# Optimization experiments

Hardware: AMD Instinct MI355X
Metric: run time of the kernel (lower is better)

## Reference

```python
import jax, jax.numpy as jnp
import numpy as np

D_MODEL = 2048
NUM_HEADS = 16
D_K = D_MODEL // NUM_HEADS


def setup_inputs() -> dict:
    key = jax.random.key(0)
    ks = jax.random.split(key, 9)
    s = 1.0 / np.sqrt(D_MODEL)
    x = jax.random.normal(ks[0], (4, 4096, D_MODEL), dtype=jnp.float32)
    wq = jax.random.uniform(ks[1], (D_MODEL, D_MODEL), jnp.float32, -s, s)
    bq = jax.random.uniform(ks[2], (D_MODEL,), jnp.float32, -s, s)
    wk = jax.random.uniform(ks[3], (D_MODEL, D_MODEL), jnp.float32, -s, s)
    bk = jax.random.uniform(ks[4], (D_MODEL,), jnp.float32, -s, s)
    wv = jax.random.uniform(ks[5], (D_MODEL, D_MODEL), jnp.float32, -s, s)
    bv = jax.random.uniform(ks[6], (D_MODEL,), jnp.float32, -s, s)
    wo = jax.random.uniform(ks[7], (D_MODEL, D_MODEL), jnp.float32, -s, s)
    bo = jax.random.uniform(ks[8], (D_MODEL,), jnp.float32, -s, s)
    return {"x": x, "wq": wq, "bq": bq, "wk": wk, "bk": bk,
            "wv": wv, "bv": bv, "wo": wo, "bo": bo}


def _heads(t, B, S):
    # (B, S, d_model) -> (B, H, S, d_k)
    return t.reshape(B, S, NUM_HEADS, D_K).transpose(0, 2, 1, 3)


def reference(x, wq, bq, wk, bk, wv, bv, wo, bo):
    B, S, _ = x.shape
    Q = _heads(x @ wq.T + bq, B, S)
    K = _heads(x @ wk.T + bk, B, S)
    V = _heads(x @ wv.T + bv, B, S)
    # elu(x)+1 feature map
    Q = jax.nn.elu(Q) + 1.0
    K = jax.nn.elu(K) + 1.0
    # KV: (B,H,d_k,d_k)
    KV = jnp.einsum('bhsd,bhse->bhde', K, V)
    QKV = jnp.einsum('bhsd,bhde->bhse', Q, KV)
    K_sum = jnp.sum(K, axis=-2)                      # (B,H,d_k)
    QK_sum = jnp.einsum('bhsd,bhd->bhs', Q, K_sum)   # (B,H,S)
    out = QKV / (QK_sum[..., None] + 1e-8)
    out = out.transpose(0, 2, 1, 3).reshape(B, S, D_MODEL)
    return out @ wo.T + bo
```

## Files before the change

### kernel.cpp

```cpp
#include <hip/hip_runtime.h>


#define D_MODEL 2048
#define SEQ     4096
#define BATCH   4
#define HEADS   16
#define DKH     128
#define M_TOK   16384
#define NBH     64

using frag8 = __attribute__((ext_vector_type(8))) short;
using f32x4 = __attribute__((ext_vector_type(4))) float;

typedef __attribute__((address_space(1))) const unsigned int g_u32;
typedef __attribute__((address_space(3))) unsigned int       l_u32;

__device__ __forceinline__ unsigned short f2bf(float f) {
  unsigned u = __float_as_uint(f);
  u = u + 0x7fffu + ((u >> 16) & 1u);
  return (unsigned short)(u >> 16);
}
__device__ __forceinline__ float bf2f(unsigned short h) {
  return __uint_as_float(((unsigned)h) << 16);
}

__global__ __launch_bounds__(256) void convert_f2bf_kernel(
    const float* __restrict__ in, unsigned short* __restrict__ out, int n4) {
  int i = blockIdx.x * 256 + threadIdx.x;
  if (i < n4) {
    float4 v = reinterpret_cast<const float4*>(in)[i];
    ushort4 o;
    o.x = f2bf(v.x); o.y = f2bf(v.y); o.z = f2bf(v.z); o.w = f2bf(v.w);
    reinterpret_cast<ushort4*>(out)[i] = o;
  }
}


#define ST_B(GB, LD, SLOT, KC)                                                \
  _Pragma("unroll") for (int j_ = 0; j_ < 2; ++j_)                            \
    __builtin_amdgcn_global_load_lds(                                         \
        (g_u32*)((GB) + (srow + wid * 16 + j_ * 8 + (lane >> 3)) * (LD)       \
                 + (KC) + scg * 8),                                           \
        (l_u32*)(sh + (SLOT) * 16384 + 8192 + (wid * 16 + j_ * 8) * 64),      \
        16, 0, 0);

#define ST_A(GA, LD, SP, ST, KC)                                              \
    __builtin_amdgcn_global_load_lds(                                         \
        (g_u32*)((GA) + (srow + (ST) * 32 + (wid & 3) * 8 + (lane >> 3)) * (LD) \
                 + (KC) + (wid >> 2) * 32 + scg * 8),                         \
        (l_u32*)(sh + ((SP) + (wid >> 2)) * 16384 +                           \
                 ((ST) * 32 + (wid & 3) * 8) * 64),                           \
        16, 0, 0);

#define RD_A(S0, S1, Q)                                                       \
  a0[0] = *(const frag8*)(lds + (S0) * 16384 + tA + (Q) * 2048);              \
  a0[1] = *(const frag8*)(lds + (S0) * 16384 + tA + (Q) * 2048 + 1024);       \
  a1[0] = *(const frag8*)(lds + (S1) * 16384 + tA + (Q) * 2048);              \
  a1[1] = *(const frag8*)(lds + (S1) * 16384 + tA + (Q) * 2048 + 1024);

#define RD_B(D0, D1, S0, S1)                                                  \
  _Pragma("unroll") for (int n_ = 0; n_ < 4; ++n_) {                          \
    D0[n_] = *(const frag8*)(lds + (S0) * 16384 + tB + n_ * 1024);            \
    D1[n_] = *(const frag8*)(lds + (S1) * 16384 + tB + n_ * 1024);            \
  }

#define MM8(AQ, B0, B1)                                                       \
  __builtin_amdgcn_s_setprio(1);                                              \
  _Pragma("unroll") for (int j_ = 0; j_ < 2; ++j_)                            \
  _Pragma("unroll") for (int n_ = 0; n_ < 4; ++n_)                            \
    acc[(AQ) + j_][n_] = __builtin_amdgcn_mfma_f32_16x16x32_bf16(             \
        a0[j_], B0[n_], acc[(AQ) + j_][n_], 0, 0, 0);                         \
  _Pragma("unroll") for (int j_ = 0; j_ < 2; ++j_)                            \
  _Pragma("unroll") for (int n_ = 0; n_ < 4; ++n_)                            \
    acc[(AQ) + j_][n_] = __builtin_amdgcn_mfma_f32_16x16x32_bf16(             \
        a1[j_], B1[n_], acc[(AQ) + j_][n_], 0, 0, 0);                         \
  __builtin_amdgcn_s_setprio(0);

#define BAR __builtin_amdgcn_s_barrier()
#define LG0                                                                   \
  asm volatile("s_waitcnt lgkmcnt(0)" ::: "memory");                          \
  __builtin_amdgcn_sched_barrier(0)

template <int MODE, bool XMAJOR>
__global__ __launch_bounds__(512, 2) void gemm256_nt_kernel(
    const unsigned short* __restrict__ A, long lda,
    const unsigned short* __restrict__ Bm, long ldb,
    void* __restrict__ Cv, long ldc,
    const float* __restrict__ bias, float* __restrict__ aux,
    float* __restrict__ qsum, int K) {
  __shared__ unsigned short sh[65536];
  const int lane = threadIdx.x & 63, wid = threadIdx.x >> 6;
  const int wm = wid >> 2, wn = wid & 3;
  const int lr = lane & 15, lh = lane >> 4;

  const int gx = gridDim.x, gy = gridDim.y;
  const int cpx = (gx * gy) >> 3;
  const int P = blockIdx.y * gx + blockIdx.x;
  const int Lw = (P & 7) * cpx + (P >> 3);
  int bx, by;
  if (XMAJOR) { bx = Lw / gy; by = Lw - bx * gy; }
  else        { by = Lw / gx; bx = Lw - by * gx; }

  const long m0 = (long)by * 256, n0 = (long)bx * 256;
  const unsigned short* Ablk = A + m0 * lda;
  const unsigned short* Bblk = Bm + n0 * ldb;
  const int NT = K >> 6;

  const int qA = (wm * 4 + lh) ^ (lr & 7);
  const int qB = ((wn >> 1) * 4 + lh) ^ (lr & 7);
  const unsigned short* lds = sh;
  const int tA = lr * 64 + qA * 8;
  const int tB = 8192 + ((wn & 1) * 64 + lr) * 64 + qB * 8;

  const int sqd = (lane & 7) ^ (lane >> 3);
  const int scg = sqd & 3;
  const long srow = (long)((sqd >> 2) * 128);

  f32x4 acc[8][4];
#pragma unroll
  for (int m = 0; m < 8; ++m)
#pragma unroll
    for (int n = 0; n < 4; ++n) acc[m][n] = (f32x4){0.f, 0.f, 0.f, 0.f};

  frag8 a0[2], a1[2], bu0[4], bu1[4], bv0[4], bv1[4];

  ST_B(Bblk, ldb, 0, 0)
  ST_B(Bblk, ldb, 1, 32)
  ST_A(Ablk, lda, 0, 0, 0) ST_A(Ablk, lda, 0, 1, 0)
  ST_A(Ablk, lda, 0, 2, 0) ST_A(Ablk, lda, 0, 3, 0)
  if (NT > 1) {
    ST_B(Bblk, ldb, 2, 64)
    ST_B(Bblk, ldb, 3, 96)
    ST_A(Ablk, lda, 2, 0, 64) ST_A(Ablk, lda, 2, 1, 64)
  }
  asm volatile("s_waitcnt vmcnt(6)" ::: "memory");
  BAR;

  const int NI = NT >> 1;
  for (int i = 0; i < NI; ++i) {
    const int kv = i * 128 + 64, kw = i * 128 + 128, kx = i * 128 + 192;
    const bool wok = (i + 1) < NI;
    RD_A(0, 1, 0)
    RD_B(bu0, bu1, 0, 1)
    ST_A(Ablk, lda, 2, 2, kv) ST_A(Ablk, lda, 2, 3, kv)
    asm volatile("s_waitcnt lgkmcnt(8)" ::: "memory");
    BAR; LG0;
    MM8(0, bu0, bu1)
    BAR;
    RD_A(0, 1, 1)
    if (wok) { ST_B(Bblk, ldb, 0, kw) }
    BAR; LG0;
    MM8(2, bu0, bu1)
    BAR;
    RD_A(0, 1, 2)
    if (wok) { ST_B(Bblk, ldb, 1, kw + 32) }
    BAR; LG0;
    MM8(4, bu0, bu1)
    BAR;
    RD_A(0, 1, 3)
    if (wok) { ST_A(Ablk, lda, 0, 0, kw) ST_A(Ablk, lda, 0, 1, kw) }
    if (wok) asm volatile("s_waitcnt vmcnt(6)" ::: "memory");
    else     asm volatile("s_waitcnt vmcnt(0)" ::: "memory");
    BAR; LG0;
    MM8(6, bu0, bu1)
    BAR;
    RD_A(2, 3, 0)
    RD_B(bv0, bv1, 2, 3)
    if (wok) { ST_A(Ablk, lda, 0, 2, kw) ST_A(Ablk, lda, 0, 3, kw) }
    asm volatile("s_waitcnt lgkmcnt(8)" ::: "memory");
    BAR; LG0;
    MM8(0, bv0, bv1)
    BAR;
    RD_A(2, 3, 1)
    if (wok) { ST_B(Bblk, ldb, 2, kx) }
    BAR; LG0;
    MM8(2, bv0, bv1)
    BAR;
    RD_A(2, 3, 2)
    if (wok) { ST_B(Bblk, ldb, 3, kx + 32) }
    BAR; LG0;
    MM8(4, bv0, bv1)
    BAR;
    RD_A(2, 3, 3)
    if (wok) { ST_A(Ablk, lda, 2, 0, kx) ST_A(Ablk, lda, 2, 1, kx)
               asm volatile("s_waitcnt vmcnt(6)" ::: "memory"); }
    BAR; LG0;
    MM8(6, bv0, bv1)
    BAR;
  }

  float* red = (float*)sh;
  if (MODE == 0 || MODE == 1) {
    if (threadIdx.x < 512) { red[threadIdx.x] = 0.f; }
    __syncthreads();
  }
  float ksv[4];
  if (MODE == 0) {
    const long b2048 = (m0 >> 12) * 2048;
#pragma unroll
    for (int n = 0; n < 4; ++n)
      ksv[n] = aux[b2048 + n0 + wn * 64 + n * 16 + lr];
  }
#pragma unroll
  for (int m = 0; m < 8; ++m)
#pragma unroll
    for (int r = 0; r < 4; ++r) {
      const int lrow = wm * 128 + (m >> 1) * 32 + (m & 1) * 16 + lh * 4 + r;
      const long row = m0 + lrow;
      float part = 0.f;
#pragma unroll
      for (int n = 0; n < 4; ++n) {
        long col = n0 + wn * 64 + n * 16 + lr;
        float v = acc[m][n][r];
        if (MODE == 0) {
          v += bias[col]; v = v > 0.f ? v + 1.f : __expf(v);
          unsigned short us = f2bf(v);
          ((unsigned short*)Cv)[row * ldc + col] = us;
          part += bf2f(us) * ksv[n];
        } else if (MODE == 1) {
          v += bias[row]; v = v > 0.f ? v + 1.f : __expf(v);
          unsigned short us = f2bf(v);
          ((unsigned short*)Cv)[row * ldc + col] = us;
          part += bf2f(us);
        } else if (MODE == 2) {
          v += bias[row];
          ((unsigned short*)Cv)[row * ldc + col] = f2bf(v);
        } else {
          v += bias[col];
          ((float*)Cv)[row * ldc + col] = v;
        }
      }
      if (MODE == 0 || MODE == 1) {
#pragma unroll
        for (int s = 1; s < 16; s <<= 1) part += __shfl_xor(part, s);
        if (lr == 0) {
          if (MODE == 0) atomicAdd(&red[lrow * 2 + (wn >> 1)], part);
          else           atomicAdd(&red[lrow], part);
        }
      }
    }
  if (MODE == 0) {
    __syncthreads();
    if (threadIdx.x < 512) {
      const int lrow = threadIdx.x >> 1, hh = threadIdx.x & 1;
      const long grow = m0 + lrow;
      qsum[((grow >> 12) * 16 + (n0 >> 7) + hh) * (long)SEQ + (grow & 4095)] =
          red[threadIdx.x];
    }
  } else if (MODE == 1) {
    __syncthreads();
    if (threadIdx.x < 256)
      atomicAdd(&aux[(n0 >> 12) * 2048 + m0 + threadIdx.x], red[threadIdx.x]);
  }
}

__device__ __forceinline__ void stage_tile(const unsigned short* __restrict__ G,
                                           long ld, unsigned short* __restrict__ L) {
  const int w = threadIdx.x >> 6, l = threadIdx.x & 63;
#pragma unroll
  for (int r = 0; r < 4; ++r) {
    const int chunk = w * 4 + r;
    const int row = chunk * 8 + (l >> 3);
    const int col = (l & 7) * 8;
    __builtin_amdgcn_global_load_lds((g_u32*)(G + (long)row * ld + col),
                                     (l_u32*)(L + chunk * 512), 16, 0, 0);
  }
}

__device__ __forceinline__ void gemm_mainloop(const unsigned short* __restrict__ A, long lda,
                                              const unsigned short* __restrict__ B, long ldb,
                                              int K, unsigned short* lA, unsigned short* lB,
                                              f32x4 acc[4][4]) {
  const int lane = threadIdx.x & 63;
  const int wid  = threadIdx.x >> 6;
  const int wr = wid >> 1, wc = wid & 1;
  const int lr = lane & 15, lh = lane >> 4;
  for (int k0 = 0; k0 < K; k0 += 64) {
    stage_tile(A + k0, lda, lA);
    stage_tile(B + k0, ldb, lB);
    __syncthreads();
#pragma unroll
    for (int kk = 0; kk < 64; kk += 32) {
      frag8 av[4], bv[4];
#pragma unroll
      for (int m = 0; m < 4; ++m)
        av[m] = *reinterpret_cast<const frag8*>(lA + (wr * 64 + m * 16 + lr) * 64 + kk + lh * 8);
#pragma unroll
      for (int n = 0; n < 4; ++n)
        bv[n] = *reinterpret_cast<const frag8*>(lB + (wc * 64 + n * 16 + lr) * 64 + kk + lh * 8);
#pragma unroll
      for (int m = 0; m < 4; ++m)
#pragma unroll
        for (int n = 0; n < 4; ++n)
          acc[m][n] = __builtin_amdgcn_mfma_f32_16x16x32_bf16(av[m], bv[n], acc[m][n], 0, 0, 0);
    }
    __syncthreads();
  }
}

#define ACC_INIT(acc)                                   \
  _Pragma("unroll") for (int m_ = 0; m_ < 4; ++m_)      \
  _Pragma("unroll") for (int n_ = 0; n_ < 4; ++n_)      \
      acc[m_][n_] = (f32x4){0.f, 0.f, 0.f, 0.f};

__global__ __launch_bounds__(256) void kvt_partial_kernel(
    const unsigned short* __restrict__ VT, const unsigned short* __restrict__ KT,
    float* __restrict__ part) {
  __shared__ unsigned short lA[128 * 64], lB[128 * 64];
  const int z = blockIdx.x;
  const int bh = z >> 3, c = z & 7;
  const int b = bh >> 4, h = bh & 15;
  const long tOff = (long)b * SEQ + (long)c * 512;
  const unsigned short* A  = VT + (long)(h * DKH) * M_TOK + tOff;
  const unsigned short* Bm = KT + (long)(h * DKH) * M_TOK + tOff;
  f32x4 acc[4][4];
  ACC_INIT(acc);
  gemm_mainloop(A, M_TOK, Bm, M_TOK, 512, lA, lB, acc);
  const int lane = threadIdx.x & 63, wid = threadIdx.x >> 6;
  const int wr = wid >> 1, wc = wid & 1, lr = lane & 15, lh = lane >> 4;
  float* out = part + (long)z * (DKH * DKH);
#pragma unroll
  for (int m = 0; m < 4; ++m)
#pragma unroll
    for (int n = 0; n < 4; ++n)
#pragma unroll
      for (int r = 0; r < 4; ++r) {
        int row = wr * 64 + m * 16 + lh * 4 + r;
        int col = wc * 64 + n * 16 + lr;
        out[row * DKH + col] = acc[m][n][r];
      }
}

__global__ __launch_bounds__(256) void reduce_kvt_kernel(
    const float* __restrict__ part, unsigned short* __restrict__ kvt) {
  int i = blockIdx.x * 256 + threadIdx.x;
  if (i < NBH * DKH * DKH) {
    int bh = i >> 14, j = i & 16383;
    float s = 0.f;
#pragma unroll
    for (int c = 0; c < 8; ++c) s += part[(((long)bh * 8 + c) << 14) + j];
    kvt[i] = f2bf(s);
  }
}

__global__ __launch_bounds__(256) void qkv_kernel(const unsigned short* __restrict__ Q,
                                                  const unsigned short* __restrict__ KVT,
                                                  const float* __restrict__ qsum,
                                                  unsigned short* __restrict__ attn) {
  __shared__ unsigned short lA[128 * 64], lB[128 * 64];
  const int z = blockIdx.z, b = z >> 4, h = z & 15;
  const long m0 = (long)blockIdx.y * 128;
  const unsigned short* A  = Q + ((long)b * SEQ + m0) * D_MODEL + h * DKH;
  const unsigned short* Bm = KVT + (long)z * (DKH * DKH);
  f32x4 acc[4][4];
  ACC_INIT(acc);
  gemm_mainloop(A, D_MODEL, Bm, DKH, DKH, lA, lB, acc);
  const int lane = threadIdx.x & 63, wid = threadIdx.x >> 6;
  const int wr = wid >> 1, wc = wid & 1, lr = lane & 15, lh = lane >> 4;
#pragma unroll
  for (int m = 0; m < 4; ++m)
#pragma unroll
    for (int n = 0; n < 4; ++n)
#pragma unroll
      for (int r = 0; r < 4; ++r) {
        long row = m0 + wr * 64 + m * 16 + lh * 4 + r;
        int  col = wc * 64 + n * 16 + lr;
        float dnm = qsum[(long)z * SEQ + row] + 1e-8f;
        float v = acc[m][n][r] / dnm;
        attn[((long)b * SEQ + row) * D_MODEL + h * DKH + col] = f2bf(v);
      }
}

#define OFF_XB   0L
#define OFF_WQ   (OFF_XB + (long)M_TOK * D_MODEL * 2)
#define OFF_WK   (OFF_WQ + (long)D_MODEL * D_MODEL * 2)
#define OFF_WV   (OFF_WK + (long)D_MODEL * D_MODEL * 2)
#define OFF_WO   (OFF_WV + (long)D_MODEL * D_MODEL * 2)
#define OFF_QB   (OFF_WO + (long)D_MODEL * D_MODEL * 2)
#define OFF_KT   (OFF_QB + (long)M_TOK * D_MODEL * 2)
#define OFF_VT   (OFF_KT + (long)M_TOK * D_MODEL * 2)
#define OFF_PART (OFF_VT + (long)M_TOK * D_MODEL * 2)
#define OFF_KVT  (OFF_PART + (long)512 * DKH * DKH * 4)
#define OFF_KSUM (OFF_KVT + (long)NBH * DKH * DKH * 2)
#define OFF_QSUM (OFF_KSUM + (long)NBH * DKH * 4)
#define OFF_ATTN OFF_XB

extern "C" void kernel_launch(void* const* d_in, const int* in_sizes, int n_in,
                              void* d_out, int out_size, void* d_ws, size_t ws_size,
                              hipStream_t stream) {
  const float* x  = (const float*)d_in[0];
  const float* wq = (const float*)d_in[1];
  const float* bq = (const float*)d_in[2];
  const float* wk = (const float*)d_in[3];
  const float* bk = (const float*)d_in[4];
  const float* wv = (const float*)d_in[5];
  const float* bv = (const float*)d_in[6];
  const float* wo = (const float*)d_in[7];
  const float* bo = (const float*)d_in[8];

  char* ws = (char*)d_ws;
  unsigned short* xb   = (unsigned short*)(ws + OFF_XB);
  unsigned short* wqb  = (unsigned short*)(ws + OFF_WQ);
  unsigned short* wkb  = (unsigned short*)(ws + OFF_WK);
  unsigned short* wvb  = (unsigned short*)(ws + OFF_WV);
  unsigned short* wob  = (unsigned short*)(ws + OFF_WO);
  unsigned short* Qb   = (unsigned short*)(ws + OFF_QB);
  unsigned short* KTb  = (unsigned short*)(ws + OFF_KT);
  unsigned short* VTb  = (unsigned short*)(ws + OFF_VT);
  float*          part = (float*)(ws + OFF_PART);
  unsigned short* KVTb = (unsigned short*)(ws + OFF_KVT);
  float*          ksum = (float*)(ws + OFF_KSUM);
  float*          qsum = (float*)(ws + OFF_QSUM);
  unsigned short* attn = (unsigned short*)(ws + OFF_ATTN);

  dim3 blk(256);
  dim3 blk5(512);

  convert_f2bf_kernel<<<(M_TOK * D_MODEL / 4) / 256, blk, 0, stream>>>(x, xb, M_TOK * D_MODEL / 4);
  convert_f2bf_kernel<<<(D_MODEL * D_MODEL / 4) / 256, blk, 0, stream>>>(wq, wqb, D_MODEL * D_MODEL / 4);
  convert_f2bf_kernel<<<(D_MODEL * D_MODEL / 4) / 256, blk, 0, stream>>>(wk, wkb, D_MODEL * D_MODEL / 4);
  convert_f2bf_kernel<<<(D_MODEL * D_MODEL / 4) / 256, blk, 0, stream>>>(wv, wvb, D_MODEL * D_MODEL / 4);
  convert_f2bf_kernel<<<(D_MODEL * D_MODEL / 4) / 256, blk, 0, stream>>>(wo, wob, D_MODEL * D_MODEL / 4);

  hipMemsetAsync(ksum, 0, NBH * DKH * sizeof(float), stream);

  gemm256_nt_kernel<1, true><<<dim3(M_TOK / 256, D_MODEL / 256), blk5, 0, stream>>>(
      wkb, D_MODEL, xb, D_MODEL, KTb, M_TOK, bk, ksum, nullptr, D_MODEL);
  gemm256_nt_kernel<0, false><<<dim3(D_MODEL / 256, M_TOK / 256), blk5, 0, stream>>>(
      xb, D_MODEL, wqb, D_MODEL, Qb, D_MODEL, bq, ksum, qsum, D_MODEL);
  gemm256_nt_kernel<2, true><<<dim3(M_TOK / 256, D_MODEL / 256), blk5, 0, stream>>>(
      wvb, D_MODEL, xb, D_MODEL, VTb, M_TOK, bv, nullptr, nullptr, D_MODEL);

  kvt_partial_kernel<<<512, blk, 0, stream>>>(VTb, KTb, part);
  reduce_kvt_kernel<<<(NBH * DKH * DKH) / 256, blk, 0, stream>>>(part, KVTb);

  qkv_kernel<<<dim3(1, SEQ / 128, NBH), blk, 0, stream>>>(Qb, KVTb, qsum, attn);

  gemm256_nt_kernel<3, false><<<dim3(D_MODEL / 256, M_TOK / 256), blk5, 0, stream>>>(
      attn, D_MODEL, wob, D_MODEL, d_out, D_MODEL, bo, nullptr, nullptr, D_MODEL);
}
```

Before: 668.3 us.

## Move Q·Ksum denominator from Q-projection epilogue into qkv kernel

```diff
diff --git a/kernel.cpp b/kernel.cpp
--- a/kernel.cpp
+++ b/kernel.cpp
@@ -86,8 +86,7 @@
     const unsigned short* __restrict__ A, long lda,
     const unsigned short* __restrict__ Bm, long ldb,
     void* __restrict__ Cv, long ldc,
-    const float* __restrict__ bias, float* __restrict__ aux,
-    float* __restrict__ qsum, int K) {
+    const float* __restrict__ bias, float* __restrict__ aux, int K) {
   __shared__ unsigned short sh[65536];
   const int lane = threadIdx.x & 63, wid = threadIdx.x >> 6;
   const int wm = wid >> 2, wn = wid & 3;
@@ -189,68 +188,54 @@
     BAR;
   }
 
-  float* red = (float*)sh;
-  if (MODE == 0 || MODE == 1) {
-    if (threadIdx.x < 512) { red[threadIdx.x] = 0.f; }
-    __syncthreads();
-  }
-  float ksv[4];
-  if (MODE == 0) {
-    const long b2048 = (m0 >> 12) * 2048;
-#pragma unroll
-    for (int n = 0; n < 4; ++n)
-      ksv[n] = aux[b2048 + n0 + wn * 64 + n * 16 + lr];
-  }
-#pragma unroll
-  for (int m = 0; m < 8; ++m)
-#pragma unroll
-    for (int r = 0; r < 4; ++r) {
-      const int lrow = wm * 128 + (m >> 1) * 32 + (m & 1) * 16 + lh * 4 + r;
-      const long row = m0 + lrow;
-      float part = 0.f;
-#pragma unroll
-      for (int n = 0; n < 4; ++n) {
-        long col = n0 + wn * 64 + n * 16 + lr;
-        float v = acc[m][n][r];
-        if (MODE == 0) {
-          v += bias[col]; v = v > 0.f ? v + 1.f : __expf(v);
-          unsigned short us = f2bf(v);
-          ((unsigned short*)Cv)[row * ldc + col] = us;
-          part += bf2f(us) * ksv[n];
-        } else if (MODE == 1) {
-          v += bias[row]; v = v > 0.f ? v + 1.f : __expf(v);
+  if constexpr (MODE == 1) {
+    __shared__ float red2[256];
+    if (threadIdx.x < 256) red2[threadIdx.x] = 0.f;
+    __syncthreads();
+#pragma unroll
+    for (int m = 0; m < 8; ++m)
+#pragma unroll
+      for (int r = 0; r < 4; ++r) {
+        const int lrow = wm * 128 + (m >> 1) * 32 + (m & 1) * 16 + lh * 4 + r;
+        const long row = m0 + lrow;
+        float part = 0.f;
+#pragma unroll
+        for (int n = 0; n < 4; ++n) {
+          long col = n0 + wn * 64 + n * 16 + lr;
+          float v = acc[m][n][r] + bias[row];
+          v = v > 0.f ? v + 1.f : __expf(v);
           unsigned short us = f2bf(v);
           ((unsigned short*)Cv)[row * ldc + col] = us;
           part += bf2f(us);
-        } else if (MODE == 2) {
-          v += bias[row];
-          ((unsigned short*)Cv)[row * ldc + col] = f2bf(v);
-        } else {
-          v += bias[col];
-          ((float*)Cv)[row * ldc + col] = v;
         }
+#pragma unroll
+        for (int s = 1; s < 16; s <<= 1) part += __shfl_xor(part, s);
+        if (lr == 0) atomicAdd(&red2[lrow], part);
       }
-      if (MODE == 0 || MODE == 1) {
-#pragma unroll
-        for (int s = 1; s < 16; s <<= 1) part += __shfl_xor(part, s);
-        if (lr == 0) {
-          if (MODE == 0) atomicAdd(&red[lrow * 2 + (wn >> 1)], part);
-          else           atomicAdd(&red[lrow], part);
+    __syncthreads();
+    if (threadIdx.x < 256)
+      atomicAdd(&aux[(n0 >> 12) * 2048 + m0 + threadIdx.x], red2[threadIdx.x]);
+  } else {
+#pragma unroll
+    for (int m = 0; m < 8; ++m)
+#pragma unroll
+      for (int n = 0; n < 4; ++n)
+#pragma unroll
+        for (int r = 0; r < 4; ++r) {
+          long row = m0 + wm * 128 + (m >> 1) * 32 + (m & 1) * 16 + lh * 4 + r;
+          long col = n0 + wn * 64 + n * 16 + lr;
+          float v = acc[m][n][r];
+          if (MODE == 0) {
+            v += bias[col]; v = v > 0.f ? v + 1.f : __expf(v);
+            ((unsigned short*)Cv)[row * ldc + col] = f2bf(v);
+          } else if (MODE == 2) {
+            v += bias[row];
+            ((unsigned short*)Cv)[row * ldc + col] = f2bf(v);
+          } else {
+            v += bias[col];
+            ((float*)Cv)[row * ldc + col] = v;
+          }
         }
-      }
-    }
-  if (MODE == 0) {
-    __syncthreads();
-    if (threadIdx.x < 512) {
-      const int lrow = threadIdx.x >> 1, hh = threadIdx.x & 1;
-      const long grow = m0 + lrow;
-      qsum[((grow >> 12) * 16 + (n0 >> 7) + hh) * (long)SEQ + (grow & 4095)] =
-          red[threadIdx.x];
-    }
-  } else if (MODE == 1) {
-    __syncthreads();
-    if (threadIdx.x < 256)
-      atomicAdd(&aux[(n0 >> 12) * 2048 + m0 + threadIdx.x], red[threadIdx.x]);
   }
 }
 
@@ -345,27 +330,65 @@
 
 __global__ __launch_bounds__(256) void qkv_kernel(const unsigned short* __restrict__ Q,
                                                   const unsigned short* __restrict__ KVT,
-                                                  const float* __restrict__ qsum,
+                                                  const float* __restrict__ ksum,
                                                   unsigned short* __restrict__ attn) {
   __shared__ unsigned short lA[128 * 64], lB[128 * 64];
+  __shared__ float qs[128];
   const int z = blockIdx.z, b = z >> 4, h = z & 15;
   const long m0 = (long)blockIdx.y * 128;
   const unsigned short* A  = Q + ((long)b * SEQ + m0) * D_MODEL + h * DKH;
   const unsigned short* Bm = KVT + (long)z * (DKH * DKH);
+  const float* ks = ksum + (long)b * 2048 + h * DKH;
   f32x4 acc[4][4];
   ACC_INIT(acc);
-  gemm_mainloop(A, D_MODEL, Bm, DKH, DKH, lA, lB, acc);
   const int lane = threadIdx.x & 63, wid = threadIdx.x >> 6;
   const int wr = wid >> 1, wc = wid & 1, lr = lane & 15, lh = lane >> 4;
+  const int qrow = threadIdx.x >> 1, qhalf = threadIdx.x & 1;
+  float qacc = 0.f;
+  for (int k0 = 0; k0 < DKH; k0 += 64) {
+    stage_tile(A + k0, D_MODEL, lA);
+    stage_tile(Bm + k0, DKH, lB);
+    __syncthreads();
+    {
+      const unsigned* pr = (const unsigned*)(lA + qrow * 64 + qhalf * 32);
+      const float* kk = ks + k0 + qhalf * 32;
+#pragma unroll
+      for (int j = 0; j < 16; ++j) {
+        unsigned u = pr[j];
+        qacc += bf2f((unsigned short)(u & 0xffff)) * kk[2 * j] +
+                bf2f((unsigned short)(u >> 16)) * kk[2 * j + 1];
+      }
+    }
+#pragma unroll
+    for (int kk2 = 0; kk2 < 64; kk2 += 32) {
+      frag8 av[4], bv[4];
+#pragma unroll
+      for (int m = 0; m < 4; ++m)
+        av[m] = *reinterpret_cast<const frag8*>(lA + (wr * 64 + m * 16 + lr) * 64 + kk2 + lh * 8);
+#pragma unroll
+      for (int n = 0; n < 4; ++n)
+        bv[n] = *reinterpret_cast<const frag8*>(lB + (wc * 64 + n * 16 + lr) * 64 + kk2 + lh * 8);
+#pragma unroll
+      for (int m = 0; m < 4; ++m)
+#pragma unroll
+        for (int n = 0; n < 4; ++n)
+          acc[m][n] = __builtin_amdgcn_mfma_f32_16x16x32_bf16(av[m], bv[n], acc[m][n], 0, 0, 0);
+    }
+    __syncthreads();
+  }
+  qacc += __shfl_xor(qacc, 1);
+  if (qhalf == 0) qs[qrow] = qacc;
+  __syncthreads();
 #pragma unroll
   for (int m = 0; m < 4; ++m)
 #pragma unroll
     for (int n = 0; n < 4; ++n)
 #pragma unroll
       for (int r = 0; r < 4; ++r) {
-        long row = m0 + wr * 64 + m * 16 + lh * 4 + r;
+        const int lrow = wr * 64 + m * 16 + lh * 4 + r;
+        long row = m0 + lrow;
         int  col = wc * 64 + n * 16 + lr;
-        float dnm = qsum[(long)z * SEQ + row] + 1e-8f;
+        float dnm = qs[lrow] + 1e-8f;
         float v = acc[m][n][r] / dnm;
         attn[((long)b * SEQ + row) * D_MODEL + h * DKH + col] = f2bf(v);
       }
@@ -410,7 +433,6 @@
   float*          part = (float*)(ws + OFF_PART);
   unsigned short* KVTb = (unsigned short*)(ws + OFF_KVT);
   float*          ksum = (float*)(ws + OFF_KSUM);
-  float*          qsum = (float*)(ws + OFF_QSUM);
   unsigned short* attn = (unsigned short*)(ws + OFF_ATTN);
 
   dim3 blk(256);
@@ -424,18 +446,18 @@
 
   hipMemsetAsync(ksum, 0, NBH * DKH * sizeof(float), stream);
 
+  gemm256_nt_kernel<0, false><<<dim3(D_MODEL / 256, M_TOK / 256), blk5, 0, stream>>>(
+      xb, D_MODEL, wqb, D_MODEL, Qb, D_MODEL, bq, nullptr, D_MODEL);
   gemm256_nt_kernel<1, true><<<dim3(M_TOK / 256, D_MODEL / 256), blk5, 0, stream>>>(
-      wkb, D_MODEL, xb, D_MODEL, KTb, M_TOK, bk, ksum, nullptr, D_MODEL);
-  gemm256_nt_kernel<0, false><<<dim3(D_MODEL / 256, M_TOK / 256), blk5, 0, stream>>>(
-      xb, D_MODEL, wqb, D_MODEL, Qb, D_MODEL, bq, ksum, qsum, D_MODEL);
+      wkb, D_MODEL, xb, D_MODEL, KTb, M_TOK, bk, ksum, D_MODEL);
   gemm256_nt_kernel<2, true><<<dim3(M_TOK / 256, D_MODEL / 256), blk5, 0, stream>>>(
-      wvb, D_MODEL, xb, D_MODEL, VTb, M_TOK, bv, nullptr, nullptr, D_MODEL);
+      wvb, D_MODEL, xb, D_MODEL, VTb, M_TOK, bv, nullptr, D_MODEL);
 
   kvt_partial_kernel<<<512, blk, 0, stream>>>(VTb, KTb, part);
   reduce_kvt_kernel<<<(NBH * DKH * DKH) / 256, blk, 0, stream>>>(part, KVTb);
 
-  qkv_kernel<<<dim3(1, SEQ / 128, NBH), blk, 0, stream>>>(Qb, KVTb, qsum, attn);
+  qkv_kernel<<<dim3(1, SEQ / 128, NBH), blk, 0, stream>>>(Qb, KVTb, ksum, attn);
 
   gemm256_nt_kernel<3, false><<<dim3(D_MODEL / 256, M_TOK / 256), blk5, 0, stream>>>(
-      attn, D_MODEL, wob, D_MODEL, d_out, D_MODEL, bo, nullptr, nullptr, D_MODEL);
-}
+      attn, D_MODEL, wob, D_MODEL, d_out, D_MODEL, bo, nullptr, D_MODEL);
+}
```

After: 662.7 us. About the same (-0.8%).
